# Performance work log

Hardware: AMD Instinct MI355X
Metric: run time of the kernel (lower is better)

Reference implementation:

```python
import jax, jax.numpy as jnp
import numpy as np
import math

H = 16
LN_EPS = 1e-5


def setup_inputs() -> dict:
    key = jax.random.key(0)
    ks = jax.random.split(key, 12)
    D = 1024
    F = T = 2048
    S = 512
    inp = {
        "hidden_states": jax.random.normal(ks[0], (S, D), jnp.float32),
        "fpos": jax.random.randint(ks[1], (F,), 0, 512, jnp.int64 if jax.config.jax_enable_x64 else jnp.int32).astype(jnp.int32),
        "tpos": jax.random.randint(ks[2], (T,), 0, 512, jnp.int32),
        "Wq": jax.random.normal(ks[3], (D, D), jnp.float32) * 0.02,
        "Wk": jax.random.normal(ks[4], (D, D), jnp.float32) * 0.02,
        "Wcb": jax.random.normal(ks[5], (D, H), jnp.float32) * 0.02,
        "Wv": jax.random.normal(ks[6], (D, D), jnp.float32) * 0.02,
        "bv": jnp.zeros((D,), jnp.float32),
        "mixing": jax.random.normal(ks[7], (H, D), jnp.float32) * 0.2,
        "Wd": jax.random.normal(ks[8], (D, D), jnp.float32) * 0.02,
        "bd": jnp.zeros((D,), jnp.float32),
        "ln_gamma": jnp.ones((D,), jnp.float32),
        "ln_beta": jnp.zeros((D,), jnp.float32),
    }
    return inp


def reference(hidden_states, fpos, tpos, Wq, Wk, Wcb, Wv, bv, mixing, Wd, bd, ln_gamma, ln_beta):
    D = hidden_states.shape[-1]
    Dh = D // H
    scale = 1.0 / math.sqrt(D / H)  # attention_head_size = dim_key_query_all / num_heads

    fidx = fpos % 512
    tidx = tpos % 512
    from_seq = hidden_states[fidx]            # [F, D]
    to_seq = hidden_states[tidx]              # [T, D]

    q = from_seq @ Wq                          # [F, D]
    k = to_seq @ Wk                            # [T, D]

    # per-head query mixing: mixed_query[h, f, d] = q[f, d] * mixing[h, d]
    mixed_q = q[None, :, :] * mixing[:, None, :]          # [H, F, D]
    scores = jnp.einsum('hfd,td->hft', mixed_q, k)        # [H, F, T]

    # content bias: [T, H] -> broadcast over queries as [H, 1, T]
    cb = (to_seq @ Wcb).T                                 # [H, T]
    scores = (scores + cb[:, None, :]) * scale

    probs = jax.nn.softmax(scores, axis=-1)               # [H, F, T]

    v = (to_seq @ Wv + bv).reshape(-1, H, Dh).transpose(1, 0, 2)  # [H, T, Dh]
    ctx = jnp.matmul(probs, v)                             # [H, F, Dh]
    ctx = ctx.transpose(1, 0, 2).reshape(-1, D)            # [F, D]

    out = ctx @ Wd + bd                                    # [F, D]
    res = from_seq + out

    mu = jnp.mean(res, axis=-1, keepdims=True)
    var = jnp.var(res, axis=-1, keepdims=True)
    normed = (res - mu) / jnp.sqrt(var + LN_EPS)
    return normed * ln_gamma + ln_beta
```

## Files before the change

### kernel.cpp

```cpp
#include <hip/hip_runtime.h>
#include <stdint.h>

typedef float  f32x4 __attribute__((ext_vector_type(4)));
typedef float  f32x2 __attribute__((ext_vector_type(2)));
typedef short  s16x8 __attribute__((ext_vector_type(8)));
typedef short  s16x4 __attribute__((ext_vector_type(4)));

__device__ __forceinline__ float bf2f(short s) {
  unsigned u = ((unsigned)(unsigned short)s) << 16;
  return __builtin_bit_cast(float, u);
}
__device__ __forceinline__ short f2bf(float f) {
  unsigned u = __builtin_bit_cast(unsigned, f);
  u = u + 0x7fffu + ((u >> 16) & 1u);
  return (short)(u >> 16);
}
__device__ __forceinline__ void g2l16(const void* g, void* l) {
  __builtin_amdgcn_global_load_lds((const __attribute__((address_space(1))) void*)g,
                                   (__attribute__((address_space(3))) void*)l,
                                   16, 0, 0);
}
#define BARRIER() do { __builtin_amdgcn_s_barrier(); __builtin_amdgcn_sched_barrier(0); } while (0)
#define VMCNT(N)  asm volatile("s_waitcnt vmcnt(" #N ")" ::: "memory")
#define MFMA(a, b, c) __builtin_amdgcn_mfma_f32_16x16x32_bf16(a, b, c, 0, 0, 0)

__global__ void wtrans_kernel(const float* __restrict__ Wq, const float* __restrict__ Wk,
                              const float* __restrict__ Wv, const float* __restrict__ Wd,
                              short* __restrict__ WqT, short* __restrict__ WkT,
                              short* __restrict__ WvT, short* __restrict__ WdT) {
  __shared__ float tile[64][65];
  const float* src; short* dst;
  switch (blockIdx.z) {
    case 0: src = Wq; dst = WqT; break;
    case 1: src = Wk; dst = WkT; break;
    case 2: src = Wv; dst = WvT; break;
    default: src = Wd; dst = WdT; break;
  }
  int k0 = blockIdx.y * 64;
  int n0 = blockIdx.x * 64;
  int tid = threadIdx.x;
#pragma unroll
  for (int p = 0; p < 4; ++p) {
    int idx = p * 1024 + tid * 4;
    int r = idx >> 6, c = idx & 63;
    f32x4 v = *(const f32x4*)(src + (size_t)(k0 + r) * 1024 + n0 + c);
    tile[r][c + 0] = v[0]; tile[r][c + 1] = v[1];
    tile[r][c + 2] = v[2]; tile[r][c + 3] = v[3];
  }
  __syncthreads();
#pragma unroll
  for (int p = 0; p < 2; ++p) {
    int idx = p * 2048 + tid * 8;
    int r = idx >> 6, c = idx & 63;
    s16x8 o;
#pragma unroll
    for (int i = 0; i < 8; ++i) o[i] = f2bf(tile[c + i][r]);
    *(s16x8*)(dst + (size_t)(n0 + r) * 1024 + k0 + c) = o;
  }
}

__global__ void smallconv_kernel(const float* __restrict__ Wcb, const float* __restrict__ mixing,
                                 short* __restrict__ WcbT, short* __restrict__ mixbf) {
  int idx = blockIdx.x * 256 + threadIdx.x;
  if (idx < 16384) {
    int h = idx >> 10, d = idx & 1023;
    WcbT[idx] = f2bf(Wcb[d * 16 + h]);
  } else {
    int j = idx - 16384;
    mixbf[j] = f2bf(mixing[j] * 0.125f);
  }
}

__global__ void gather_kernel(const float* __restrict__ hidden, const int* __restrict__ fpos,
                              const int* __restrict__ tpos, float* __restrict__ from_f,
                              short* __restrict__ from_bf, short* __restrict__ to_bf) {
  int row = blockIdx.x;
  int c = threadIdx.x * 4;
  if (blockIdx.y == 0) {
    int src = fpos[row] & 511;
    f32x4 v = *(const f32x4*)(hidden + (size_t)src * 1024 + c);
    *(f32x4*)(from_f + (size_t)row * 1024 + c) = v;
    s16x4 o;
#pragma unroll
    for (int i = 0; i < 4; ++i) o[i] = f2bf(v[i]);
    *(s16x4*)(from_bf + (size_t)row * 1024 + c) = o;
  } else {
    int src = tpos[row] & 511;
    f32x4 v = *(const f32x4*)(hidden + (size_t)src * 1024 + c);
    s16x4 o;
#pragma unroll
    for (int i = 0; i < 4; ++i) o[i] = f2bf(v[i]);
    *(s16x4*)(to_bf + (size_t)row * 1024 + c) = o;
  }
}

__global__ __launch_bounds__(256, 2)
void qkv_gemm(const short* __restrict__ from_bf, const short* __restrict__ to_bf,
              const short* __restrict__ WqT, const short* __restrict__ WkT,
              const short* __restrict__ WvT, const float* __restrict__ bv,
              short* __restrict__ q_swz, short* __restrict__ k_swz, short* __restrict__ vTs) {
  __shared__ __align__(16) short As[128][64];
  __shared__ __align__(16) short Bs[128][64];
  int mode = blockIdx.z;
  const short* A = (mode == 0) ? from_bf : to_bf;
  const short* B = (mode == 0) ? WqT : (mode == 1) ? WkT : WvT;
  int m0 = blockIdx.x * 128, n0 = blockIdx.y * 128;
  int tid = threadIdx.x;
  int w = tid >> 6, l = tid & 63;
  int wr = w >> 1, wc = w & 1;
  f32x4 acc[4][4] = {};
  for (int k0 = 0; k0 < 1024; k0 += 64) {
    __syncthreads();
#pragma unroll
    for (int i = 0; i < 4; ++i) {
      int off = i * 4096 + tid * 16;
      int r = off >> 7, cb_ = off & 127;
      g2l16(A + ((size_t)(m0 + r) << 10) + k0 + (cb_ >> 1), (short*)As + (off >> 1));
      g2l16(B + ((size_t)(n0 + r) << 10) + k0 + (cb_ >> 1), (short*)Bs + (off >> 1));
    }
    __syncthreads();
#pragma unroll
    for (int ks = 0; ks < 2; ++ks) {
      s16x8 af[4], bfr[4];
#pragma unroll
      for (int m = 0; m < 4; ++m)
        af[m] = *(const s16x8*)&As[wr * 64 + m * 16 + (l & 15)][ks * 32 + (l >> 4) * 8];
#pragma unroll
      for (int n = 0; n < 4; ++n)
        bfr[n] = *(const s16x8*)&Bs[wc * 64 + n * 16 + (l & 15)][ks * 32 + (l >> 4) * 8];
#pragma unroll
      for (int m = 0; m < 4; ++m)
#pragma unroll
        for (int n = 0; n < 4; ++n)
          acc[m][n] = MFMA(af[m], bfr[n], acc[m][n]);
    }
  }
  int lr = (l >> 4) * 4, lc = l & 15;
#pragma unroll
  for (int m = 0; m < 4; ++m)
#pragma unroll
    for (int n = 0; n < 4; ++n) {
      int row = m0 + wr * 64 + m * 16 + lr;
      int col = n0 + wc * 64 + n * 16 + lc;
      if (mode == 0) {
#pragma unroll
        for (int r = 0; r < 4; ++r) {
          int rr = row + r;
          q_swz[(size_t)rr * 1024 + (col ^ ((rr & 7) << 3))] = f2bf(acc[m][n][r]);
        }
      } else if (mode == 1) {
#pragma unroll
        for (int r = 0; r < 4; ++r) {
          int rr = row + r;
          k_swz[(size_t)rr * 1024 + (col ^ ((rr & 7) << 3))] = f2bf(acc[m][n][r]);
        }
      } else {
        float b = bv[col];
#pragma unroll
        for (int r = 0; r < 4; ++r) {
          int rr = row + r;
          int tsw = rr ^ ((col & 7) << 3);
          vTs[(size_t)col * 2048 + tsw] = f2bf(acc[m][n][r] + b);
        }
      }
    }
}

__global__ __launch_bounds__(256, 2)
void gemm_out(const short* __restrict__ A, const short* __restrict__ B,
              const float* __restrict__ bias, const float* __restrict__ resid,
              float* __restrict__ Cout) {
  __shared__ __align__(16) short As[128][64];
  __shared__ __align__(16) short Bs[128][64];
  int m0 = blockIdx.x * 128, n0 = blockIdx.y * 128;
  int tid = threadIdx.x;
  int w = tid >> 6, l = tid & 63;
  int wr = w >> 1, wc = w & 1;
  f32x4 acc[4][4] = {};
  for (int k0 = 0; k0 < 1024; k0 += 64) {
    __syncthreads();
#pragma unroll
    for (int i = 0; i < 4; ++i) {
      int off = i * 4096 + tid * 16;
      int r = off >> 7, cb_ = off & 127;
      g2l16(A + ((size_t)(m0 + r) << 10) + k0 + (cb_ >> 1), (short*)As + (off >> 1));
      g2l16(B + ((size_t)(n0 + r) << 10) + k0 + (cb_ >> 1), (short*)Bs + (off >> 1));
    }
    __syncthreads();
#pragma unroll
    for (int ks = 0; ks < 2; ++ks) {
      s16x8 af[4], bfr[4];
#pragma unroll
      for (int m = 0; m < 4; ++m)
        af[m] = *(const s16x8*)&As[wr * 64 + m * 16 + (l & 15)][ks * 32 + (l >> 4) * 8];
#pragma unroll
      for (int n = 0; n < 4; ++n)
        bfr[n] = *(const s16x8*)&Bs[wc * 64 + n * 16 + (l & 15)][ks * 32 + (l >> 4) * 8];
#pragma unroll
      for (int m = 0; m < 4; ++m)
#pragma unroll
        for (int n = 0; n < 4; ++n)
          acc[m][n] = MFMA(af[m], bfr[n], acc[m][n]);
    }
  }
  int lr = (l >> 4) * 4, lc = l & 15;
#pragma unroll
  for (int m = 0; m < 4; ++m)
#pragma unroll
    for (int n = 0; n < 4; ++n) {
      int row = m0 + wr * 64 + m * 16 + lr;
      int col = n0 + wc * 64 + n * 16 + lc;
      float b = bias[col];
#pragma unroll
      for (int r = 0; r < 4; ++r)
        Cout[(size_t)(row + r) * 1024 + col] = acc[m][n][r] + b + resid[(size_t)(row + r) * 1024 + col];
    }
}

__global__ void cb_kernel(const short* __restrict__ to_bf, const short* __restrict__ WcbT,
                          float* __restrict__ cbv) {
  __shared__ short Wl[16 * 1024];
  int tid = threadIdx.x;
  for (int i = tid; i < 2048; i += 256)
    ((s16x8*)Wl)[i] = ((const s16x8*)WcbT)[i];
  __syncthreads();
  int w = tid >> 6, l = tid & 63;
  int t = blockIdx.x * 4 + w;
  const s16x8* xr = (const s16x8*)(to_bf + ((size_t)t << 10) + l * 16);
  s16x8 x0 = xr[0], x1 = xr[1];
  float xf[16];
#pragma unroll
  for (int i = 0; i < 8; ++i) { xf[i] = bf2f(x0[i]); xf[8 + i] = bf2f(x1[i]); }
#pragma unroll
  for (int h = 0; h < 16; ++h) {
    const s16x8* wr_ = (const s16x8*)(Wl + h * 1024 + l * 16);
    s16x8 w0 = wr_[0], w1 = wr_[1];
    float acc = 0.f;
#pragma unroll
    for (int i = 0; i < 8; ++i) { acc += xf[i] * bf2f(w0[i]); acc += xf[8 + i] * bf2f(w1[i]); }
#pragma unroll
    for (int s = 32; s; s >>= 1) acc += __shfl_xor(acc, s);
    if (l == 0) cbv[(size_t)h * 2048 + t] = acc * 0.125f;
  }
}

__global__ __launch_bounds__(512, 2)
void attn_kernel(const short* __restrict__ q_swz, const short* __restrict__ k_swz,
                 const short* __restrict__ vTs, const short* __restrict__ mixbf,
                 const float* __restrict__ cbg, float* __restrict__ ctxp,
                 f32x2* __restrict__ mlb) {
  __shared__ __align__(16) char smem[120832];
  char* qmA = smem;          char* qmB = smem + 32768;
  char* ktA = smem + 65536;  char* ktB = smem + 81920;
  char* vt  = smem + 98304;
  float* cbl  = (float*)(smem + 114688);
  short* mixl = (short*)(smem + 118784);
  const int f0 = blockIdx.x * 256, h = blockIdx.y, ts = blockIdx.z;
  const int tb = ts << 10;
  const int tid = threadIdx.x, w = tid >> 6, l = tid & 63;
  const int lr = l >> 4, lc = l & 15;
  const int swz = (lc & 7) << 4;

  for (int i = tid; i < 1024; i += 512) cbl[i] = cbg[h * 2048 + tb + i];
  for (int i = tid; i < 128; i += 512)
    ((s16x8*)mixl)[i] = ((const s16x8*)(mixbf + ((size_t)h << 10)))[i];
  __syncthreads();

#define ISSUE_QK(qmb, ktb, k0e, trow0)                                                   \
  do {                                                                                   \
    _Pragma("unroll") for (int i_ = 0; i_ < 4; ++i_) {                                   \
      int off_ = i_ * 8192 + tid * 16;                                                   \
      g2l16(q_swz + ((size_t)(f0 + (off_ >> 7)) << 10) + (k0e) + ((off_ & 127) >> 1),    \
            (qmb) + off_);                                                               \
    }                                                                                    \
    _Pragma("unroll") for (int i_ = 0; i_ < 2; ++i_) {                                   \
      int off_ = i_ * 8192 + tid * 16;                                                   \
      g2l16(k_swz + ((size_t)((trow0) + (off_ >> 7)) << 10) + (k0e) + ((off_ & 127) >> 1), \
            (ktb) + off_);                                                               \
    }                                                                                    \
  } while (0)

  ISSUE_QK(qmA, ktA, 0, tb);

  float m_run[8], l_run[8];
#pragma unroll
  for (int s2 = 0; s2 < 8; ++s2) { m_run[s2] = -1e30f; l_run[s2] = 0.f; }
  f32x4 ctx[2][4] = {};

  for (int t0 = 0; t0 < 1024; t0 += 128) {
#pragma unroll
    for (int i = 0; i < 2; ++i) {
      int off = i * 8192 + tid * 16;
      g2l16(vTs + ((size_t)(h * 64 + (off >> 8)) << 11) + tb + t0 + ((off & 255) >> 1), vt + off);
    }
    f32x4 sacc[2][8] = {};
    for (int c = 0; c < 16; ++c) {
      char* qmb = (c & 1) ? qmB : qmA;
      char* ktb = (c & 1) ? ktB : ktA;
      if (c < 15) {
        ISSUE_QK((c & 1) ? qmA : qmB, (c & 1) ? ktA : ktB, (c + 1) * 64, tb + t0);
      } else if (t0 < 896) {
        ISSUE_QK(qmA, ktA, 0, tb + t0 + 128);
      }
      if (c == 0) { VMCNT(8); }
      else if (c == 15 && t0 == 896) { VMCNT(0); }
      else { VMCNT(6); }
      BARRIER();
      const int k0b = c << 7;
#pragma unroll
      for (int ks = 0; ks < 2; ++ks) {
        int xr = ks * 64 + lr * 16;
        s16x8 mx = *(const s16x8*)((char*)mixl + k0b + xr);
        float mf[8];
#pragma unroll
        for (int e = 0; e < 8; ++e) mf[e] = bf2f(mx[e]);
        s16x8 qv = *(const s16x8*)(qmb + ((w * 32 + lc) << 7) + (xr ^ swz));
        s16x8 qw = *(const s16x8*)(qmb + ((w * 32 + 16 + lc) << 7) + (xr ^ swz));
        s16x8 af0, af1;
#pragma unroll
        for (int e = 0; e < 8; ++e) {
          af0[e] = f2bf(bf2f(qv[e]) * mf[e]);
          af1[e] = f2bf(bf2f(qw[e]) * mf[e]);
        }
        __builtin_amdgcn_s_setprio(1);
#pragma unroll
        for (int n = 0; n < 8; ++n) {
          s16x8 bfr = *(const s16x8*)(ktb + ((n * 16 + lc) << 7) + (xr ^ swz));
          sacc[0][n] = MFMA(af0, bfr, sacc[0][n]);
          sacc[1][n] = MFMA(af1, bfr, sacc[1][n]);
        }
        __builtin_amdgcn_s_setprio(0);
      }
      BARRIER();
    }
    float pm[8];
#pragma unroll
    for (int s2 = 0; s2 < 8; ++s2) pm[s2] = -1e30f;
#pragma unroll
    for (int m = 0; m < 2; ++m)
#pragma unroll
      for (int n = 0; n < 8; ++n) {
        float cbv = cbl[t0 + n * 16 + lc];
#pragma unroll
        for (int r = 0; r < 4; ++r) {
          float s = sacc[m][n][r] + cbv;
          sacc[m][n][r] = s;
          pm[m * 4 + r] = fmaxf(pm[m * 4 + r], s);
        }
      }
#pragma unroll
    for (int s_ = 1; s_ < 16; s_ <<= 1)
#pragma unroll
      for (int s2 = 0; s2 < 8; ++s2) pm[s2] = fmaxf(pm[s2], __shfl_xor(pm[s2], s_));
    float tsum[8];
#pragma unroll
    for (int s2 = 0; s2 < 8; ++s2) {
      float mnew = fmaxf(m_run[s2], pm[s2]);
      float corr = __expf(m_run[s2] - mnew);
      m_run[s2] = mnew; l_run[s2] *= corr; tsum[s2] = 0.f;
      int m = s2 >> 2, r = s2 & 3;
#pragma unroll
      for (int n2 = 0; n2 < 4; ++n2) ctx[m][n2][r] *= corr;
    }
#pragma unroll
    for (int m = 0; m < 2; ++m)
#pragma unroll
      for (int n = 0; n < 8; ++n)
#pragma unroll
        for (int r = 0; r < 4; ++r) {
          float e = __expf(sacc[m][n][r] - m_run[m * 4 + r]);
          sacc[m][n][r] = e;
          tsum[m * 4 + r] += e;
        }
#pragma unroll
    for (int s_ = 1; s_ < 16; s_ <<= 1)
#pragma unroll
      for (int s2 = 0; s2 < 8; ++s2) tsum[s2] += __shfl_xor(tsum[s2], s_);
#pragma unroll
    for (int s2 = 0; s2 < 8; ++s2) l_run[s2] += tsum[s2];
    char* ptw = qmB + w * 4096;
#pragma unroll
    for (int hh = 0; hh < 2; ++hh) {
#pragma unroll
      for (int m = 0; m < 2; ++m)
#pragma unroll
        for (int nn = 0; nn < 4; ++nn)
#pragma unroll
          for (int r = 0; r < 4; ++r) {
            int row = m * 16 + lr * 4 + r;
            *(short*)(ptw + (row << 7) + ((((nn * 16 + lc) << 1)) ^ ((row & 7) << 4))) =
                f2bf(sacc[m][hh * 4 + nn][r]);
          }
#pragma unroll
      for (int ks = 0; ks < 2; ++ks) {
        s16x8 paf0 = *(const s16x8*)(ptw + (lc << 7) + ((ks * 64 + lr * 16) ^ swz));
        s16x8 paf1 = *(const s16x8*)(ptw + ((16 + lc) << 7) + ((ks * 64 + lr * 16) ^ swz));
#pragma unroll
        for (int n2 = 0; n2 < 4; ++n2) {
          s16x8 vb = *(const s16x8*)(vt + ((n2 * 16 + lc) << 8) +
                                     ((hh * 128 + ks * 64 + lr * 16) ^ swz));
          ctx[0][n2] = MFMA(paf0, vb, ctx[0][n2]);
          ctx[1][n2] = MFMA(paf1, vb, ctx[1][n2]);
        }
      }
    }
    BARRIER();
  }
  const int pb = (h * 2 + ts) * 2048;
#pragma unroll
  for (int m = 0; m < 2; ++m)
#pragma unroll
    for (int n2 = 0; n2 < 4; ++n2)
#pragma unroll
      for (int r = 0; r < 4; ++r) {
        int f = f0 + w * 32 + m * 16 + lr * 4 + r;
        ctxp[((size_t)(pb + f) << 6) + n2 * 16 + lc] = ctx[m][n2][r];
      }
  if (lc == 0) {
#pragma unroll
    for (int s2 = 0; s2 < 8; ++s2) {
      int f = f0 + w * 32 + (s2 >> 2) * 16 + lr * 4 + (s2 & 3);
      f32x2 v; v[0] = m_run[s2]; v[1] = l_run[s2];
      mlb[pb + f] = v;
    }
  }
#undef ISSUE_QK
}

__global__ void combine_kernel(const float* __restrict__ ctxp, const f32x2* __restrict__ mlb,
                               short* __restrict__ ctx_bf) {
  int f = blockIdx.x, tid = threadIdx.x;
  int h = tid >> 4, d4 = (tid & 15) * 4;
  f32x2 a = mlb[(h * 2 + 0) * 2048 + f];
  f32x2 b = mlb[(h * 2 + 1) * 2048 + f];
  float m = fmaxf(a[0], b[0]);
  float e0 = __expf(a[0] - m), e1 = __expf(b[0] - m);
  float inv = 1.f / (a[1] * e0 + b[1] * e1);
  f32x4 c0 = *(const f32x4*)(ctxp + (((size_t)(h * 2 + 0) * 2048 + f) << 6) + d4);
  f32x4 c1 = *(const f32x4*)(ctxp + (((size_t)(h * 2 + 1) * 2048 + f) << 6) + d4);
  s16x4 o;
#pragma unroll
  for (int i = 0; i < 4; ++i) o[i] = f2bf((c0[i] * e0 + c1[i] * e1) * inv);
  *(s16x4*)(ctx_bf + ((size_t)f << 10) + h * 64 + d4) = o;
}

__global__ void ln_kernel(const float* __restrict__ res, const float* __restrict__ gamma,
                          const float* __restrict__ beta, float* __restrict__ out) {
  int row = blockIdx.x, tid = threadIdx.x;
  f32x4 x = *(const f32x4*)(res + ((size_t)row << 10) + tid * 4);
  float s = x[0] + x[1] + x[2] + x[3];
  float s2 = x[0] * x[0] + x[1] * x[1] + x[2] * x[2] + x[3] * x[3];
#pragma unroll
  for (int m = 1; m < 64; m <<= 1) { s += __shfl_xor(s, m); s2 += __shfl_xor(s2, m); }
  __shared__ float red[8];
  int w = tid >> 6, l = tid & 63;
  if (l == 0) { red[w] = s; red[4 + w] = s2; }
  __syncthreads();
  s = red[0] + red[1] + red[2] + red[3];
  s2 = red[4] + red[5] + red[6] + red[7];
  float mu = s * (1.f / 1024.f);
  float var = s2 * (1.f / 1024.f) - mu * mu;
  float rstd = rsqrtf(var + 1e-5f);
  f32x4 o;
#pragma unroll
  for (int i = 0; i < 4; ++i)
    o[i] = (x[i] - mu) * rstd * gamma[tid * 4 + i] + beta[tid * 4 + i];
  *(f32x4*)(out + ((size_t)row << 10) + tid * 4) = o;
}

extern "C" void kernel_launch(void* const* d_in, const int* in_sizes, int n_in,
                              void* d_out, int out_size, void* d_ws, size_t ws_size,
                              hipStream_t stream) {
  const float* hidden = (const float*)d_in[0];
  const int*   fpos   = (const int*)d_in[1];
  const int*   tpos   = (const int*)d_in[2];
  const float* Wq     = (const float*)d_in[3];
  const float* Wk     = (const float*)d_in[4];
  const float* Wcb    = (const float*)d_in[5];
  const float* Wv     = (const float*)d_in[6];
  const float* bv     = (const float*)d_in[7];
  const float* mixing = (const float*)d_in[8];
  const float* Wd     = (const float*)d_in[9];
  const float* bd     = (const float*)d_in[10];
  const float* gamma  = (const float*)d_in[11];
  const float* beta   = (const float*)d_in[12];

  char* p = (char*)d_ws;
  auto alloc = [&](size_t bytes) { char* r = p; p += (bytes + 255) & ~(size_t)255; return r; };
  float* from_f  = (float*)alloc((size_t)2048 * 1024 * 4);
  short* from_bf = (short*)alloc((size_t)2048 * 1024 * 2);
  short* to_bf   = (short*)alloc((size_t)2048 * 1024 * 2);
  short* WqT     = (short*)alloc((size_t)1024 * 1024 * 2);
  short* WkT     = (short*)alloc((size_t)1024 * 1024 * 2);
  short* WvT     = (short*)alloc((size_t)1024 * 1024 * 2);
  short* WdT     = (short*)alloc((size_t)1024 * 1024 * 2);
  short* WcbT    = (short*)alloc((size_t)16 * 1024 * 2);
  short* mixbf   = (short*)alloc((size_t)16 * 1024 * 2);
  short* q_swz   = (short*)alloc((size_t)2048 * 1024 * 2);
  short* k_swz   = (short*)alloc((size_t)2048 * 1024 * 2);
  short* vTs     = (short*)alloc((size_t)1024 * 2048 * 2);
  float* cbb     = (float*)alloc((size_t)16 * 2048 * 4);
  short* ctx_bf  = (short*)alloc((size_t)2048 * 1024 * 2);
  float* ctxp    = (float*)alloc((size_t)32 * 2048 * 64 * 4);
  f32x2* mlb     = (f32x2*)alloc((size_t)32 * 2048 * 8);

  wtrans_kernel<<<dim3(16, 16, 4), 256, 0, stream>>>(Wq, Wk, Wv, Wd, WqT, WkT, WvT, WdT);
  smallconv_kernel<<<128, 256, 0, stream>>>(Wcb, mixing, WcbT, mixbf);
  gather_kernel<<<dim3(2048, 2), 256, 0, stream>>>(hidden, fpos, tpos, from_f, from_bf, to_bf);
  qkv_gemm<<<dim3(16, 8, 3), 256, 0, stream>>>(from_bf, to_bf, WqT, WkT, WvT, bv,
                                               q_swz, k_swz, vTs);
  cb_kernel<<<512, 256, 0, stream>>>(to_bf, WcbT, cbb);
  attn_kernel<<<dim3(8, 16, 2), 512, 0, stream>>>(q_swz, k_swz, vTs, mixbf, cbb, ctxp, mlb);
  combine_kernel<<<2048, 256, 0, stream>>>(ctxp, mlb, ctx_bf);
  gemm_out<<<dim3(16, 8), 256, 0, stream>>>(ctx_bf, WdT, bd, from_f, (float*)d_out);
  ln_kernel<<<2048, 256, 0, stream>>>((float*)d_out, gamma, beta, (float*)d_out);
}
```

Before: 394.3 us.

## Precompute per-head mixed queries and switch softmax to exp2 with folded log2e

Adds a qmix kernel that writes per-head mixed queries (q*mixing, swizzled) to a 64MB workspace buffer, so the attention inner loop loads ready-made MFMA operands instead of multiplying and converting them on every chunk. The softmax scale now folds in log2(e), which lets exp2f replace __expf in attention and combine. The in-kernel fallback path uses the packed bf16 convert instruction. The cost is an extra pass that writes and later re-reads 64MB of mixed queries, and it only runs when the workspace is large enough.

```diff
diff --git a/kernel.cpp b/kernel.cpp
--- a/kernel.cpp
+++ b/kernel.cpp
@@ -1,10 +1,14 @@
 #include <hip/hip_runtime.h>
 #include <stdint.h>
-
-typedef float  f32x4 __attribute__((ext_vector_type(4)));
-typedef float  f32x2 __attribute__((ext_vector_type(2)));
-typedef short  s16x8 __attribute__((ext_vector_type(8)));
-typedef short  s16x4 __attribute__((ext_vector_type(4)));
+#include <math.h>
+
+typedef float    f32x4 __attribute__((ext_vector_type(4)));
+typedef float    f32x2 __attribute__((ext_vector_type(2)));
+typedef short    s16x8 __attribute__((ext_vector_type(8)));
+typedef short    s16x4 __attribute__((ext_vector_type(4)));
+typedef unsigned u32x4 __attribute__((ext_vector_type(4)));
+
+#define SCALE_LOG2E 0.1803368751839806f
 
 __device__ __forceinline__ float bf2f(short s) {
   unsigned u = ((unsigned)(unsigned short)s) << 16;
@@ -14,6 +18,11 @@
   unsigned u = __builtin_bit_cast(unsigned, f);
   u = u + 0x7fffu + ((u >> 16) & 1u);
   return (short)(u >> 16);
+}
+__device__ __forceinline__ unsigned cvtpk(float lo, float hi) {
+  unsigned r;
+  asm("v_cvt_pk_bf16_f32 %0, %1, %2" : "=v"(r) : "v"(lo), "v"(hi));
+  return r;
 }
 __device__ __forceinline__ void g2l16(const void* g, void* l) {
   __builtin_amdgcn_global_load_lds((const __attribute__((address_space(1))) void*)g,
@@ -67,7 +76,7 @@
     WcbT[idx] = f2bf(Wcb[d * 16 + h]);
   } else {
     int j = idx - 16384;
-    mixbf[j] = f2bf(mixing[j] * 0.125f);
+    mixbf[j] = f2bf(mixing[j] * SCALE_LOG2E);
   }
 }
 
@@ -240,12 +249,28 @@
     for (int i = 0; i < 8; ++i) { acc += xf[i] * bf2f(w0[i]); acc += xf[8 + i] * bf2f(w1[i]); }
 #pragma unroll
     for (int s = 32; s; s >>= 1) acc += __shfl_xor(acc, s);
-    if (l == 0) cbv[(size_t)h * 2048 + t] = acc * 0.125f;
-  }
-}
-
+    if (l == 0) cbv[(size_t)h * 2048 + t] = acc * SCALE_LOG2E;
+  }
+}
+
+__global__ void qmix_kernel(const short* __restrict__ q_swz, const short* __restrict__ mixbf,
+                            short* __restrict__ qmix) {
+  int f = blockIdx.x, h = blockIdx.y;
+  int c = threadIdx.x * 8;
+  int fs = (f & 7) << 3;
+  s16x8 qv = *(const s16x8*)(q_swz + ((size_t)f << 10) + c);
+  s16x8 mv = *(const s16x8*)(mixbf + ((size_t)h << 10) + (c ^ fs));
+  u32x4 o;
+#pragma unroll
+  for (int e2 = 0; e2 < 4; ++e2)
+    o[e2] = cvtpk(bf2f(qv[2 * e2]) * bf2f(mv[2 * e2]),
+                  bf2f(qv[2 * e2 + 1]) * bf2f(mv[2 * e2 + 1]));
+  *(s16x8*)(qmix + (((size_t)h * 2048 + f) << 10) + c) = __builtin_bit_cast(s16x8, o);
+}
+
+template <bool QMIX>
 __global__ __launch_bounds__(512, 2)
-void attn_kernel(const short* __restrict__ q_swz, const short* __restrict__ k_swz,
+void attn_kernel(const short* __restrict__ qsrc, const short* __restrict__ k_swz,
                  const short* __restrict__ vTs, const short* __restrict__ mixbf,
                  const float* __restrict__ cbg, float* __restrict__ ctxp,
                  f32x2* __restrict__ mlb) {
@@ -262,22 +287,26 @@
   const int swz = (lc & 7) << 4;
 
   for (int i = tid; i < 1024; i += 512) cbl[i] = cbg[h * 2048 + tb + i];
-  for (int i = tid; i < 128; i += 512)
-    ((s16x8*)mixl)[i] = ((const s16x8*)(mixbf + ((size_t)h << 10)))[i];
+  if (!QMIX)
+    for (int i = tid; i < 128; i += 512)
+      ((s16x8*)mixl)[i] = ((const s16x8*)(mixbf + ((size_t)h << 10)))[i];
   __syncthreads();
 
-#define ISSUE_QK(qmb, ktb, k0e, trow0)                                                   \
-  do {                                                                                   \
-    _Pragma("unroll") for (int i_ = 0; i_ < 4; ++i_) {                                   \
-      int off_ = i_ * 8192 + tid * 16;                                                   \
-      g2l16(q_swz + ((size_t)(f0 + (off_ >> 7)) << 10) + (k0e) + ((off_ & 127) >> 1),    \
-            (qmb) + off_);                                                               \
-    }                                                                                    \
-    _Pragma("unroll") for (int i_ = 0; i_ < 2; ++i_) {                                   \
-      int off_ = i_ * 8192 + tid * 16;                                                   \
+  const short* qrow = QMIX ? qsrc + (((size_t)h * 2048 + f0) << 10)
+                           : qsrc + ((size_t)f0 << 10);
+
+#define ISSUE_QK(qmb, ktb, k0e, trow0)                                                     \
+  do {                                                                                     \
+    _Pragma("unroll") for (int i_ = 0; i_ < 4; ++i_) {                                     \
+      int off_ = i_ * 8192 + tid * 16;                                                     \
+      g2l16(qrow + ((size_t)(off_ >> 7) << 10) + (k0e) + ((off_ & 127) >> 1),              \
+            (qmb) + off_);                                                                 \
+    }                                                                                      \
+    _Pragma("unroll") for (int i_ = 0; i_ < 2; ++i_) {                                     \
+      int off_ = i_ * 8192 + tid * 16;                                                     \
       g2l16(k_swz + ((size_t)((trow0) + (off_ >> 7)) << 10) + (k0e) + ((off_ & 127) >> 1), \
-            (ktb) + off_);                                                               \
-    }                                                                                    \
+            (ktb) + off_);                                                                 \
+    }                                                                                      \
   } while (0)
 
   ISSUE_QK(qmA, ktA, 0, tb);
@@ -310,17 +339,23 @@
 #pragma unroll
       for (int ks = 0; ks < 2; ++ks) {
         int xr = ks * 64 + lr * 16;
-        s16x8 mx = *(const s16x8*)((char*)mixl + k0b + xr);
-        float mf[8];
-#pragma unroll
-        for (int e = 0; e < 8; ++e) mf[e] = bf2f(mx[e]);
-        s16x8 qv = *(const s16x8*)(qmb + ((w * 32 + lc) << 7) + (xr ^ swz));
-        s16x8 qw = *(const s16x8*)(qmb + ((w * 32 + 16 + lc) << 7) + (xr ^ swz));
         s16x8 af0, af1;
-#pragma unroll
-        for (int e = 0; e < 8; ++e) {
-          af0[e] = f2bf(bf2f(qv[e]) * mf[e]);
-          af1[e] = f2bf(bf2f(qw[e]) * mf[e]);
+        if (QMIX) {
+          af0 = *(const s16x8*)(qmb + ((w * 32 + lc) << 7) + (xr ^ swz));
+          af1 = *(const s16x8*)(qmb + ((w * 32 + 16 + lc) << 7) + (xr ^ swz));
+        } else {
+          s16x8 mx = *(const s16x8*)((char*)mixl + k0b + xr);
+          s16x8 qv = *(const s16x8*)(qmb + ((w * 32 + lc) << 7) + (xr ^ swz));
+          s16x8 qw = *(const s16x8*)(qmb + ((w * 32 + 16 + lc) << 7) + (xr ^ swz));
+          u32x4 a0u, a1u;
+#pragma unroll
+          for (int e2 = 0; e2 < 4; ++e2) {
+            float m0 = bf2f(mx[2 * e2]), m1 = bf2f(mx[2 * e2 + 1]);
+            a0u[e2] = cvtpk(bf2f(qv[2 * e2]) * m0, bf2f(qv[2 * e2 + 1]) * m1);
+            a1u[e2] = cvtpk(bf2f(qw[2 * e2]) * m0, bf2f(qw[2 * e2 + 1]) * m1);
+          }
+          af0 = __builtin_bit_cast(s16x8, a0u);
+          af1 = __builtin_bit_cast(s16x8, a1u);
         }
         __builtin_amdgcn_s_setprio(1);
 #pragma unroll
@@ -356,7 +391,7 @@
 #pragma unroll
     for (int s2 = 0; s2 < 8; ++s2) {
       float mnew = fmaxf(m_run[s2], pm[s2]);
-      float corr = __expf(m_run[s2] - mnew);
+      float corr = exp2f(m_run[s2] - mnew);
       m_run[s2] = mnew; l_run[s2] *= corr; tsum[s2] = 0.f;
       int m = s2 >> 2, r = s2 & 3;
 #pragma unroll
@@ -368,7 +403,7 @@
       for (int n = 0; n < 8; ++n)
 #pragma unroll
         for (int r = 0; r < 4; ++r) {
-          float e = __expf(sacc[m][n][r] - m_run[m * 4 + r]);
+          float e = exp2f(sacc[m][n][r] - m_run[m * 4 + r]);
           sacc[m][n][r] = e;
           tsum[m * 4 + r] += e;
         }
@@ -434,7 +469,7 @@
   f32x2 a = mlb[(h * 2 + 0) * 2048 + f];
   f32x2 b = mlb[(h * 2 + 1) * 2048 + f];
   float m = fmaxf(a[0], b[0]);
-  float e0 = __expf(a[0] - m), e1 = __expf(b[0] - m);
+  float e0 = exp2f(a[0] - m), e1 = exp2f(b[0] - m);
   float inv = 1.f / (a[1] * e0 + b[1] * e1);
   f32x4 c0 = *(const f32x4*)(ctxp + (((size_t)(h * 2 + 0) * 2048 + f) << 6) + d4);
   f32x4 c1 = *(const f32x4*)(ctxp + (((size_t)(h * 2 + 1) * 2048 + f) << 6) + d4);
@@ -503,6 +538,9 @@
   short* ctx_bf  = (short*)alloc((size_t)2048 * 1024 * 2);
   float* ctxp    = (float*)alloc((size_t)32 * 2048 * 64 * 4);
   f32x2* mlb     = (f32x2*)alloc((size_t)32 * 2048 * 8);
+  size_t used = (size_t)(p - (char*)d_ws);
+  short* qmixb = (short*)p;
+  bool use_qmix = ws_size >= used + (size_t)16 * 2048 * 1024 * 2;
 
   wtrans_kernel<<<dim3(16, 16, 4), 256, 0, stream>>>(Wq, Wk, Wv, Wd, WqT, WkT, WvT, WdT);
   smallconv_kernel<<<128, 256, 0, stream>>>(Wcb, mixing, WcbT, mixbf);
@@ -510,7 +548,12 @@
   qkv_gemm<<<dim3(16, 8, 3), 256, 0, stream>>>(from_bf, to_bf, WqT, WkT, WvT, bv,
                                                q_swz, k_swz, vTs);
   cb_kernel<<<512, 256, 0, stream>>>(to_bf, WcbT, cbb);
-  attn_kernel<<<dim3(8, 16, 2), 512, 0, stream>>>(q_swz, k_swz, vTs, mixbf, cbb, ctxp, mlb);
+  if (use_qmix) {
+    qmix_kernel<<<dim3(2048, 16), 128, 0, stream>>>(q_swz, mixbf, qmixb);
+    attn_kernel<true><<<dim3(8, 16, 2), 512, 0, stream>>>(qmixb, k_swz, vTs, mixbf, cbb, ctxp, mlb);
+  } else {
+    attn_kernel<false><<<dim3(8, 16, 2), 512, 0, stream>>>(q_swz, k_swz, vTs, mixbf, cbb, ctxp, mlb);
+  }
   combine_kernel<<<2048, 256, 0, stream>>>(ctxp, mlb, ctx_bf);
   gemm_out<<<dim3(16, 8), 256, 0, stream>>>(ctx_bf, WdT, bd, from_f, (float*)d_out);
   ln_kernel<<<2048, 256, 0, stream>>>((float*)d_out, gamma, beta, (float*)d_out);
```

Result: faster. 350.7 us (-11.0%).
